# Kernel tuning notes

Hardware: AMD Instinct MI355X
Metric: run time of the kernel (lower is better)

## Reference

```python
import jax, jax.numpy as jnp
import numpy as np

N, E, F, H, C, G, NC = 50000, 800000, 128, 3, 64, 16, 10
NEG_SLOPE = 0.2


def gatv2_layer(x, src, dst, Wl, Wr, att, b, concat):
    # PyG GATv2Conv (share_weights=False, add_self_loops already in src/dst)
    n = x.shape[0]
    h, c = att.shape
    xl = (x @ Wl).reshape(n, h, c)   # source-side transform
    xr = (x @ Wr).reshape(n, h, c)   # target-side transform
    # per-edge attention logits: a^T LeakyReLU(xl_j + xr_i)
    e = jax.nn.leaky_relu(xl[src] + xr[dst], NEG_SLOPE)          # [E,h,c]
    logits = jnp.einsum('ehc,hc->eh', e, att)                    # [E,h]
    # segment softmax over incoming edges of each target node
    m = jax.ops.segment_max(logits, dst, num_segments=n)
    m = jnp.where(jnp.isfinite(m), m, jnp.zeros_like(m))
    p = jnp.exp(logits - m[dst])
    denom = jax.ops.segment_sum(p, dst, num_segments=n)
    alpha = p / jnp.maximum(denom[dst], 1e-16)                   # [E,h]
    out = jax.ops.segment_sum(alpha[:, :, None] * xl[src], dst, num_segments=n)
    out = out.reshape(n, h * c) if concat else out.mean(axis=1)
    return out + b


def setup_inputs() -> dict:
    key = jax.random.key(0)
    ks = jax.random.split(key, 16)
    glorot = lambda k, shp: jax.random.normal(k, shp, jnp.float32) * np.sqrt(2.0 / (shp[0] + shp[-1]))
    return {
        'x': jax.random.normal(ks[0], (N, F), jnp.float32),
        'edge_index': jax.random.randint(ks[1], (2, E), 0, N, jnp.int64),
        'batch': jnp.sort(jax.random.randint(ks[2], (N,), 0, G, jnp.int64)),
        'Wl1': glorot(ks[3], (F, H * C)),
        'Wr1': glorot(ks[4], (F, H * C)),
        'att1': glorot(ks[5], (H, C)),
        'b1': jnp.zeros((H * C,), jnp.float32),
        'Wl2': glorot(ks[6], (H * C, H * C)),
        'Wr2': glorot(ks[7], (H * C, H * C)),
        'att2': glorot(ks[8], (H, C)),
        'b2': jnp.zeros((C,), jnp.float32),
        'Wc': glorot(ks[9], (C, NC)),
        'bc': jnp.zeros((NC,), jnp.float32),
    }


def reference(x, edge_index, batch, Wl1, Wr1, att1, b1, Wl2, Wr2, att2, b2, Wc, bc):
    n = x.shape[0]
    loops = jnp.arange(n, dtype=edge_index.dtype)
    src = jnp.concatenate([edge_index[0], loops])  # add self loops (PyG default)
    dst = jnp.concatenate([edge_index[1], loops])
    h = jax.nn.relu(gatv2_layer(x, src, dst, Wl1, Wr1, att1, b1, True))
    # dropout is identity in eval mode
    h = jax.nn.relu(gatv2_layer(h, src, dst, Wl2, Wr2, att2, b2, False))
    # global mean pool over graph ids
    sums = jax.ops.segment_sum(h, batch, num_segments=G)
    counts = jax.ops.segment_sum(jnp.ones((n, 1), h.dtype), batch, num_segments=G)
    pooled = sums / jnp.maximum(counts, 1.0)
    logits = pooled @ Wc + bc
    return jax.nn.softmax(logits, axis=1)
```

## Files before the change

kernel.cpp:

```cpp
#include <hip/hip_runtime.h>
#include <hip/hip_bf16.h>
#include <stdint.h>

#define NN 50000
#define EE 800000
#define FF 128
#define HH 3
#define CC 64
#define GG 16
#define NCLS 10
#define HC (HH*CC)

#define LOG2E 1.4426950408889634f

typedef uint16_t u16;
typedef __attribute__((ext_vector_type(8))) short short8;
typedef __attribute__((ext_vector_type(4))) float f32x4;

__device__ __forceinline__ u16 bf16_rne(float x) {
    uint32_t u = __float_as_uint(x);
    u += 0x7fffu + ((u >> 16) & 1u);
    return (u16)(u >> 16);
}
__device__ __forceinline__ void split2(float x, u16& h, u16& l) {
    h = bf16_rne(x);
    float fh = __uint_as_float((uint32_t)h << 16);
    l = bf16_rne(x - fh);
}

__device__ __forceinline__ float qsum16(float x) {
    #define DPP_ADD(ctrl) \
        x += __int_as_float(__builtin_amdgcn_update_dpp(0, __float_as_int(x), ctrl, 0xf, 0xf, true))
    DPP_ADD(0x111);
    DPP_ADD(0x112);
    DPP_ADD(0x114);
    DPP_ADD(0x118);
    #undef DPP_ADD
    return __int_as_float(__builtin_amdgcn_ds_swizzle(__float_as_int(x), 0x1F0));
}

__device__ __forceinline__ void unpack12(uint4 q0, uint2 q1, float v[3][4]) {
    v[0][0] = __uint_as_float(q0.x << 16);
    v[1][0] = __uint_as_float(q0.x & 0xffff0000u);
    v[2][0] = __uint_as_float(q0.y << 16);
    v[0][1] = __uint_as_float(q0.y & 0xffff0000u);
    v[1][1] = __uint_as_float(q0.z << 16);
    v[2][1] = __uint_as_float(q0.z & 0xffff0000u);
    v[0][2] = __uint_as_float(q0.w << 16);
    v[1][2] = __uint_as_float(q0.w & 0xffff0000u);
    v[2][2] = __uint_as_float(q1.x << 16);
    v[0][3] = __uint_as_float(q1.x & 0xffff0000u);
    v[1][3] = __uint_as_float(q1.y << 16);
    v[2][3] = __uint_as_float(q1.y & 0xffff0000u);
}

__global__ void count_deg(const int* __restrict__ dst, int* __restrict__ deg, int E) {
    int i = blockIdx.x * blockDim.x + threadIdx.x;
    if (i < E) atomicAdd(&deg[dst[i]], 1);
}

__global__ __launch_bounds__(256) void scan_local(const int* __restrict__ deg,
                                                  int* __restrict__ rowp1,
                                                  int* __restrict__ partials, int n) {
    __shared__ int sums[256];
    int base = blockIdx.x * 2048 + threadIdx.x * 8;
    int v[8]; int run = 0;
    #pragma unroll
    for (int i = 0; i < 8; ++i) {
        int x = (base + i < n) ? deg[base + i] + 1 : 0;
        run += x; v[i] = run;
    }
    sums[threadIdx.x] = run;
    __syncthreads();
    for (int off = 1; off < 256; off <<= 1) {
        int t = (threadIdx.x >= off) ? sums[threadIdx.x - off] : 0;
        __syncthreads();
        sums[threadIdx.x] += t;
        __syncthreads();
    }
    int prefix = (threadIdx.x > 0) ? sums[threadIdx.x - 1] : 0;
    #pragma unroll
    for (int i = 0; i < 8; ++i)
        if (base + i < n) rowp1[base + i] = v[i] + prefix;
    if (threadIdx.x == 255) partials[blockIdx.x] = sums[255];
}

__global__ void scan_partials(int* partials, int nb) {
    if (threadIdx.x == 0 && blockIdx.x == 0) {
        int run = 0;
        for (int b = 0; b < nb; ++b) { int t = partials[b]; partials[b] = run; run += t; }
    }
}

__global__ void scan_finish(int* __restrict__ rowp, int* __restrict__ cursor,
                            const int* __restrict__ partials, int n) {
    int i = blockIdx.x * blockDim.x + threadIdx.x;
    if (i == 0) { rowp[0] = 0; cursor[0] = 0; }
    if (i < n) {
        int v = rowp[1 + i] + partials[i / 2048];
        rowp[1 + i] = v;
        if (i < n - 1) cursor[i + 1] = v;
    }
}

__global__ void fill_csr(const int* __restrict__ src, const int* __restrict__ dst,
                         int* __restrict__ cursor, int* __restrict__ colv, int E) {
    int i = blockIdx.x * blockDim.x + threadIdx.x;
    if (i < E) {
        int pos = atomicAdd(&cursor[dst[i]], 1);
        colv[pos] = src[i];
    }
}

__global__ void add_self(const int* __restrict__ rowp, int* __restrict__ colv, int n) {
    int i = blockIdx.x * blockDim.x + threadIdx.x;
    if (i < n) colv[rowp[i + 1] - 1] = i;
}

__global__ void prep_all(const float* __restrict__ Wl1, const float* __restrict__ Wr1,
                         const float* __restrict__ Wl2, const float* __restrict__ Wr2,
                         u16* l1h, u16* l1l, u16* r1h, u16* r1l,
                         u16* l2h, u16* l2l, u16* r2h, u16* r2l) {
    int idx = blockIdx.x * blockDim.x + threadIdx.x;
    const int S1 = FF * HC, S2 = HC * HC;
    const float* B; u16 *H, *L; int K, f;
    if (idx < S1)                { B = Wl1; H = l1h; L = l1l; K = FF; f = idx; }
    else if (idx < 2*S1)         { B = Wr1; H = r1h; L = r1l; K = FF; f = idx - S1; }
    else if (idx < 2*S1 + S2)    { B = Wl2; H = l2h; L = l2l; K = HC; f = idx - 2*S1; }
    else if (idx < 2*S1 + 2*S2)  { B = Wr2; H = r2h; L = r2l; K = HC; f = idx - 2*S1 - S2; }
    else return;
    const int KB = K / 32;
    int j    = f & 7;
    int lane = (f >> 3) & 63;
    int rest = f >> 9;
    int kb    = rest % KB;
    int ntile = rest / KB;
    int n = ntile * 16 + (lane & 15);
    int k = kb * 32 + (lane >> 4) * 8 + j;
    u16 h, l; split2(B[k * HC + n], h, l);
    H[f] = h;
    L[f] = l;
}

template<int K, bool SPLITIN>
__global__ __launch_bounds__(256) void mfma_gemm(
    const float* __restrict__ Af,
    const u16* __restrict__ Ahi, const u16* __restrict__ Alo,
    const u16* __restrict__ B1h, const u16* __restrict__ B1l,
    const u16* __restrict__ B2h, const u16* __restrict__ B2l,
    u16* __restrict__ C1p, u16* __restrict__ C2p, int M)
{
    constexpr int KB  = K / 32;
    constexpr int NCH = K / 8;
    __shared__ __align__(16) u16 smem[64 * K * 2];
    u16* Ah = smem;
    u16* Al = smem + 64 * K;

    const int tid  = threadIdx.x;
    const int w    = tid >> 6;
    const int lane = tid & 63;
    const int m0   = blockIdx.x * 64;

    #pragma unroll
    for (int i = 0; i < (64 * NCH) / 256; ++i) {
        int id   = tid + 256 * i;
        int row  = id & 63;
        int c    = id >> 6;
        int rt   = row >> 4, frow = row & 15;
        int kb   = c >> 2,   fkc  = c & 3;
        int sw   = (rt ^ (rt << 1)) & 7;
        int slot = (fkc * 16 + frow) ^ sw;
        int laddr = ((rt * KB + kb) * 64 + slot) * 8;
        int grow = min(m0 + row, M - 1);
        if constexpr (SPLITIN) {
            float4 a0 = *(const float4*)(Af + (size_t)grow * K + c * 8);
            float4 a1 = *(const float4*)(Af + (size_t)grow * K + c * 8 + 4);
            ushort4 h0, l0, h1, l1;
            split2(a0.x, h0.x, l0.x); split2(a0.y, h0.y, l0.y);
            split2(a0.z, h0.z, l0.z); split2(a0.w, h0.w, l0.w);
            split2(a1.x, h1.x, l1.x); split2(a1.y, h1.y, l1.y);
            split2(a1.z, h1.z, l1.z); split2(a1.w, h1.w, l1.w);
            *(ushort4*)&Ah[laddr]     = h0;
            *(ushort4*)&Ah[laddr + 4] = h1;
            *(ushort4*)&Al[laddr]     = l0;
            *(ushort4*)&Al[laddr + 4] = l1;
        } else {
            *(uint4*)&Ah[laddr] = *(const uint4*)(Ahi + (size_t)grow * K + c * 8);
            *(uint4*)&Al[laddr] = *(const uint4*)(Alo + (size_t)grow * K + c * 8);
        }
    }
    __syncthreads();

    f32x4 acc[2][3][4];
    #pragma unroll
    for (int mt = 0; mt < 2; ++mt)
        #pragma unroll
        for (int nt = 0; nt < 3; ++nt)
            #pragma unroll
            for (int rt = 0; rt < 4; ++rt)
                acc[mt][nt][rt] = (f32x4){0.f, 0.f, 0.f, 0.f};

    const u16* bbase[2][3][2];
    #pragma unroll
    for (int mt = 0; mt < 2; ++mt) {
        const u16* Bh = mt ? B2h : B1h;
        const u16* Bl = mt ? B2l : B1l;
        #pragma unroll
        for (int nt = 0; nt < 3; ++nt) {
            size_t o = ((size_t)(w * 3 + nt) * KB * 64 + lane) * 8;
            bbase[mt][nt][0] = Bh + o;
            bbase[mt][nt][1] = Bl + o;
        }
    }

    #pragma unroll 2
    for (int kb = 0; kb < KB; ++kb) {
        short8 afh[4], afl[4];
        #pragma unroll
        for (int rt = 0; rt < 4; ++rt) {
            int sw = (rt ^ (rt << 1)) & 7;
            int laddr = ((rt * KB + kb) * 64 + (lane ^ sw)) * 8;
            afh[rt] = *(const short8*)&Ah[laddr];
            afl[rt] = *(const short8*)&Al[laddr];
        }
        #pragma unroll
        for (int mt = 0; mt < 2; ++mt) {
            #pragma unroll
            for (int nt = 0; nt < 3; ++nt) {
                short8 bh = *(const short8*)(bbase[mt][nt][0] + kb * 512);
                short8 bl = *(const short8*)(bbase[mt][nt][1] + kb * 512);
                #pragma unroll
                for (int rt = 0; rt < 4; ++rt)
                    acc[mt][nt][rt] = __builtin_amdgcn_mfma_f32_16x16x32_bf16(afh[rt], bh, acc[mt][nt][rt], 0, 0, 0);
                #pragma unroll
                for (int rt = 0; rt < 4; ++rt)
                    acc[mt][nt][rt] = __builtin_amdgcn_mfma_f32_16x16x32_bf16(afh[rt], bl, acc[mt][nt][rt], 0, 0, 0);
                #pragma unroll
                for (int rt = 0; rt < 4; ++rt)
                    acc[mt][nt][rt] = __builtin_amdgcn_mfma_f32_16x16x32_bf16(afl[rt], bh, acc[mt][nt][rt], 0, 0, 0);
            }
        }
    }

    const int frow = lane & 15;
    const int q4   = (lane >> 4) * 4;
    #pragma unroll
    for (int mt = 0; mt < 2; ++mt) {
        __syncthreads();
        #pragma unroll
        for (int nt = 0; nt < 3; ++nt) {
            int col = w * 48 + nt * 16 + frow;
            int c = col & 63, h = col >> 6;
            int u = c * 3 + h;
            int chunk = u >> 3, within = u & 7;
            #pragma unroll
            for (int rt = 0; rt < 4; ++rt)
                #pragma unroll
                for (int r = 0; r < 4; ++r) {
                    int lrow = rt * 16 + q4 + r;
                    smem[lrow * 256 + ((chunk ^ (lrow & 7)) << 3) + within] =
                        bf16_rne(acc[mt][nt][rt][r]);
                }
        }
        __syncthreads();
        u16* C = mt ? C2p : C1p;
        #pragma unroll
        for (int i = 0; i < 6; ++i) {
            int idx  = tid + 256 * i;
            int lrow = idx / 24;
            int coff = idx % 24;
            if (m0 + lrow < M)
                *(uint4*)(C + (size_t)(m0 + lrow) * HC + coff * 8) =
                    *(const uint4*)&smem[lrow * 256 + ((coff ^ (lrow & 7)) << 3)];
        }
    }
}

template<bool MASK>
__device__ __forceinline__ void gat_quad(
    int i0, int q, int l, int beg, int cnt, int cm1,
    const int* __restrict__ colv, const u16* __restrict__ xlp,
    const float attv[3][4], const float xrv[3][4],
    float s[3], float acc[3][4])
{
    int idx = i0 + q;
    int iq  = MASK ? min(idx, cm1) : idx;
    int src = colv[beg + iq];
    const u16* p = xlp + (size_t)src * HC + l * 12;
    uint4 q0 = *(const uint4*)p;
    uint2 q1 = *(const uint2*)(p + 8);
    float v[3][4];
    unpack12(q0, q1, v);
    #pragma unroll
    for (int r = 0; r < 3; ++r) {
        float t0 = v[r][0] + xrv[r][0]; t0 = fmaxf(t0, 0.2f * t0);
        float t1 = v[r][1] + xrv[r][1]; t1 = fmaxf(t1, 0.2f * t1);
        float t2 = v[r][2] + xrv[r][2]; t2 = fmaxf(t2, 0.2f * t2);
        float t3 = v[r][3] + xrv[r][3]; t3 = fmaxf(t3, 0.2f * t3);
        float d = t0 * attv[r][0];
        d = fmaf(t1, attv[r][1], d);
        d = fmaf(t2, attv[r][2], d);
        d = fmaf(t3, attv[r][3], d);
        d = qsum16(d);
        float pe = __builtin_amdgcn_exp2f(d);
        if (MASK) pe = (idx < cnt) ? pe : 0.f;
        s[r] += pe;
        acc[r][0] = fmaf(pe, v[r][0], acc[r][0]);
        acc[r][1] = fmaf(pe, v[r][1], acc[r][1]);
        acc[r][2] = fmaf(pe, v[r][2], acc[r][2]);
        acc[r][3] = fmaf(pe, v[r][3], acc[r][3]);
    }
}

template<int CONCAT>
__global__ __launch_bounds__(256) void gat_agg(
    const u16* __restrict__ xlp, const u16* __restrict__ xrp,
    const int* __restrict__ rowp, const int* __restrict__ colv,
    const float* __restrict__ att, const float* __restrict__ bias,
    float* __restrict__ out, u16* __restrict__ ohi, u16* __restrict__ olo, int n)
{
    const int wave = threadIdx.x >> 6;
    const int lane = threadIdx.x & 63;
    const int node = __builtin_amdgcn_readfirstlane(blockIdx.x * 4 + wave);
    if (node >= n) return;
    const int q = lane >> 4;
    const int l = lane & 15;

    float attv[3][4], xrv[3][4];
    #pragma unroll
    for (int r = 0; r < 3; ++r) {
        float4 a4 = *(const float4*)(att + r * 64 + 4 * l);
        attv[r][0] = a4.x * LOG2E; attv[r][1] = a4.y * LOG2E;
        attv[r][2] = a4.z * LOG2E; attv[r][3] = a4.w * LOG2E;
    }
    {
        const u16* p = xrp + (size_t)node * HC + l * 12;
        uint4 x0 = *(const uint4*)p;
        uint2 x1 = *(const uint2*)(p + 8);
        unpack12(x0, x1, xrv);
    }

    float s[3] = {0.f, 0.f, 0.f};
    float acc[3][4] = {{0.f}};

    const int beg = rowp[node];
    const int cnt = rowp[node + 1] - beg;
    const int cm1 = cnt - 1;

    int i0 = 0;
    const int nfull = cnt & ~3;
    #pragma unroll 2
    for (; i0 < nfull; i0 += 4)
        gat_quad<false>(i0, q, l, beg, cnt, cm1, colv, xlp, attv, xrv, s, acc);
    if (i0 < cnt)
        gat_quad<true>(i0, q, l, beg, cnt, cm1, colv, xlp, attv, xrv, s, acc);

    #pragma unroll
    for (int r = 0; r < 3; ++r) {
        s[r] += __shfl_xor(s[r], 16, 64);
        s[r] += __shfl_xor(s[r], 32, 64);
        #pragma unroll
        for (int j = 0; j < 4; ++j) {
            acc[r][j] += __shfl_xor(acc[r][j], 16, 64);
            acc[r][j] += __shfl_xor(acc[r][j], 32, 64);
        }
    }

    if (CONCAT) {
        if (lane < 48) {
            int r = lane >> 4, ll = lane & 15;
            float inv = 1.f / s[r];
            float4 bv = *(const float4*)(bias + r * 64 + 4 * ll);
            ushort4 hv, lv;
            float o0 = fmaxf(fmaf(acc[r][0], inv, bv.x), 0.f); split2(o0, hv.x, lv.x);
            float o1 = fmaxf(fmaf(acc[r][1], inv, bv.y), 0.f); split2(o1, hv.y, lv.y);
            float o2 = fmaxf(fmaf(acc[r][2], inv, bv.z), 0.f); split2(o2, hv.z, lv.z);
            float o3 = fmaxf(fmaf(acc[r][3], inv, bv.w), 0.f); split2(o3, hv.w, lv.w);
            size_t ob = (size_t)node * HC + r * 64 + 4 * ll;
            *(ushort4*)&ohi[ob] = hv;
            *(ushort4*)&olo[ob] = lv;
        }
    } else {
        if (lane < 16) {
            float i0v = 1.f / s[0], i1v = 1.f / s[1], i2v = 1.f / s[2];
            float4 bv = *(const float4*)(bias + 4 * l);
            float4 o;
            o.x = fmaxf((acc[0][0]*i0v + acc[1][0]*i1v + acc[2][0]*i2v) * (1.f/3.f) + bv.x, 0.f);
            o.y = fmaxf((acc[0][1]*i0v + acc[1][1]*i1v + acc[2][1]*i2v) * (1.f/3.f) + bv.y, 0.f);
            o.z = fmaxf((acc[0][2]*i0v + acc[1][2]*i1v + acc[2][2]*i2v) * (1.f/3.f) + bv.z, 0.f);
            o.w = fmaxf((acc[0][3]*i0v + acc[1][3]*i1v + acc[2][3]*i2v) * (1.f/3.f) + bv.w, 0.f);
            *(float4*)&out[(size_t)node * CC + 4 * l] = o;
        }
    }
}

#define POOL_BLOCKS 384
__global__ __launch_bounds__(256) void pool_kernel(
    const float* __restrict__ h2, const int* __restrict__ batch,
    float* __restrict__ pool, float* __restrict__ cnt, int n)
{
    const int c   = threadIdx.x & 63;
    const int sub = threadIdx.x >> 6;
    const int per = (n + gridDim.x - 1) / gridDim.x;
    const int n0  = blockIdx.x * per;
    const int n1  = min(n0 + per, n);

    float run = 0.f;
    float crun = 0.f;
    int curg = -1;
    for (int node = n0 + sub; node < n1; node += 4) {
        int g = batch[node];
        if (g != curg) {
            if (curg >= 0) {
                atomicAdd(&pool[curg * CC + c], run);
                if (c == 0) atomicAdd(&cnt[curg], crun);
            }
            run = 0.f; crun = 0.f; curg = g;
        }
        run += h2[(size_t)node * CC + c];
        crun += 1.f;
    }
    if (curg >= 0) {
        atomicAdd(&pool[curg * CC + c], run);
        if (c == 0) atomicAdd(&cnt[curg], crun);
    }
}

__global__ void head_kernel(const float* __restrict__ pool, const float* __restrict__ cnt,
                            const float* __restrict__ Wc, const float* __restrict__ bc,
                            float* __restrict__ outp) {
    __shared__ float lg[GG][NCLS];
    int t = threadIdx.x;
    if (t < GG * NCLS) {
        int g = t / NCLS, k = t % NCLS;
        float invc = 1.f / fmaxf(cnt[g], 1.f);
        float a = 0.f;
        for (int c = 0; c < CC; ++c) a += pool[g * CC + c] * Wc[c * NCLS + k];
        lg[g][k] = a * invc + bc[k];
    }
    __syncthreads();
    if (t < GG) {
        float mx = -1e30f;
        for (int k = 0; k < NCLS; ++k) mx = fmaxf(mx, lg[t][k]);
        float ssum = 0.f; float e[NCLS];
        for (int k = 0; k < NCLS; ++k) { e[k] = __expf(lg[t][k] - mx); ssum += e[k]; }
        for (int k = 0; k < NCLS; ++k) outp[t * NCLS + k] = e[k] / ssum;
    }
}

extern "C" void kernel_launch(void* const* d_in, const int* in_sizes, int n_in,
                              void* d_out, int out_size, void* d_ws, size_t ws_size,
                              hipStream_t stream) {
    const float* x     = (const float*)d_in[0];
    const int*   ei    = (const int*)d_in[1];
    const int*   batch = (const int*)d_in[2];
    const float* Wl1   = (const float*)d_in[3];
    const float* Wr1   = (const float*)d_in[4];
    const float* att1  = (const float*)d_in[5];
    const float* b1    = (const float*)d_in[6];
    const float* Wl2   = (const float*)d_in[7];
    const float* Wr2   = (const float*)d_in[8];
    const float* att2  = (const float*)d_in[9];
    const float* b2    = (const float*)d_in[10];
    const float* Wc    = (const float*)d_in[11];
    const float* bc    = (const float*)d_in[12];

    const int n = in_sizes[2];
    const int E = in_sizes[1] / 2;
    const int* srcv = ei;
    const int* dstv = ei + E;

    char* base = (char*)d_ws;
    size_t off = 0;
    auto alloc = [&](size_t bytes) -> char* {
        char* p = base + off;
        off = (off + bytes + 255) & ~(size_t)255;
        return p;
    };
    int*   deg      = (int*)  alloc((size_t)n * 4);
    int*   cursor   = (int*)  alloc((size_t)n * 4);
    int*   rowp     = (int*)  alloc((size_t)(n + 1) * 4);
    int*   partials = (int*)  alloc(256 * 4);
    int*   colv     = (int*)  alloc((size_t)(E + n) * 4);
    u16*   xlp      = (u16*)  alloc((size_t)n * HC * 2);
    u16*   xrp      = (u16*)  alloc((size_t)n * HC * 2);
    u16*   bufHi    = (u16*)  alloc((size_t)n * HC * 2);
    u16*   bufLo    = (u16*)  alloc((size_t)n * HC * 2);
    float* h2       = (float*)alloc((size_t)n * CC * 4);
    float* pool     = (float*)alloc((size_t)GG * (CC + 1) * 4);
    float* cnt      = pool + GG * CC;
    u16*   Bl1hi    = (u16*)  alloc((size_t)FF * HC * 2);
    u16*   Bl1lo    = (u16*)  alloc((size_t)FF * HC * 2);
    u16*   Br1hi    = (u16*)  alloc((size_t)FF * HC * 2);
    u16*   Br1lo    = (u16*)  alloc((size_t)FF * HC * 2);
    u16*   Bl2hi    = (u16*)  alloc((size_t)HC * HC * 2);
    u16*   Bl2lo    = (u16*)  alloc((size_t)HC * HC * 2);
    u16*   Br2hi    = (u16*)  alloc((size_t)HC * HC * 2);
    u16*   Br2lo    = (u16*)  alloc((size_t)HC * HC * 2);

    hipMemsetAsync(deg, 0, (size_t)n * 4, stream);
    count_deg<<<(E + 255) / 256, 256, 0, stream>>>(dstv, deg, E);
    int nchunks = (n + 2047) / 2048;
    scan_local<<<nchunks, 256, 0, stream>>>(deg, rowp + 1, partials, n);
    scan_partials<<<1, 64, 0, stream>>>(partials, nchunks);
    scan_finish<<<(n + 255) / 256, 256, 0, stream>>>(rowp, cursor, partials, n);
    fill_csr<<<(E + 255) / 256, 256, 0, stream>>>(srcv, dstv, cursor, colv, E);
    add_self<<<(n + 255) / 256, 256, 0, stream>>>(rowp, colv, n);

    const int prep_total = 2 * FF * HC + 2 * HC * HC;
    prep_all<<<(prep_total + 255) / 256, 256, 0, stream>>>(
        Wl1, Wr1, Wl2, Wr2, Bl1hi, Bl1lo, Br1hi, Br1lo, Bl2hi, Bl2lo, Br2hi, Br2lo);

    const int gblocks = (n + 63) / 64;

    mfma_gemm<FF, true><<<gblocks, 256, 0, stream>>>(
        x, nullptr, nullptr, Bl1hi, Bl1lo, Br1hi, Br1lo, xlp, xrp, n);
    gat_agg<1><<<(n + 3) / 4, 256, 0, stream>>>(xlp, xrp, rowp, colv, att1, b1,
                                                nullptr, bufHi, bufLo, n);

    mfma_gemm<HC, false><<<gblocks, 256, 0, stream>>>(
        nullptr, bufHi, bufLo, Bl2hi, Bl2lo, Br2hi, Br2lo, xlp, xrp, n);
    gat_agg<0><<<(n + 3) / 4, 256, 0, stream>>>(xlp, xrp, rowp, colv, att2, b2,
                                                h2, nullptr, nullptr, n);

    hipMemsetAsync(pool, 0, (size_t)GG * (CC + 1) * 4, stream);
    pool_kernel<<<POOL_BLOCKS, 256, 0, stream>>>(h2, batch, pool, cnt, n);
    head_kernel<<<1, 256, 0, stream>>>(pool, cnt, Wc, bc, (float*)d_out);
}
```

Before: 357.1 us.

## Load GEMM A fragments directly from global and halve row tile to 32

The MFMA GEMM no longer stages the A tile (hi/lo bf16 split) through shared memory. Each wave now loads its own A fragments straight from global memory into registers and splits them there. The M tile shrinks from 64 to 32 rows, which doubles the block count and cuts shared memory to the output staging buffer only. This removes the LDS staging pass and its barrier, and should raise occupancy. In exchange, all four waves redundantly read and split the same A rows, and each B fragment is reused over fewer rows.

```diff
diff --git a/kernel.cpp b/kernel.cpp
--- a/kernel.cpp
+++ b/kernel.cpp
@@ -150,57 +150,30 @@
     const u16* __restrict__ B2h, const u16* __restrict__ B2l,
     u16* __restrict__ C1p, u16* __restrict__ C2p, int M)
 {
-    constexpr int KB  = K / 32;
-    constexpr int NCH = K / 8;
-    __shared__ __align__(16) u16 smem[64 * K * 2];
-    u16* Ah = smem;
-    u16* Al = smem + 64 * K;
+    constexpr int KB = K / 32;
+    __shared__ __align__(16) u16 smem[32 * 256];
 
     const int tid  = threadIdx.x;
     const int w    = tid >> 6;
     const int lane = tid & 63;
-    const int m0   = blockIdx.x * 64;
-
-    #pragma unroll
-    for (int i = 0; i < (64 * NCH) / 256; ++i) {
-        int id   = tid + 256 * i;
-        int row  = id & 63;
-        int c    = id >> 6;
-        int rt   = row >> 4, frow = row & 15;
-        int kb   = c >> 2,   fkc  = c & 3;
-        int sw   = (rt ^ (rt << 1)) & 7;
-        int slot = (fkc * 16 + frow) ^ sw;
-        int laddr = ((rt * KB + kb) * 64 + slot) * 8;
-        int grow = min(m0 + row, M - 1);
-        if constexpr (SPLITIN) {
-            float4 a0 = *(const float4*)(Af + (size_t)grow * K + c * 8);
-            float4 a1 = *(const float4*)(Af + (size_t)grow * K + c * 8 + 4);
-            ushort4 h0, l0, h1, l1;
-            split2(a0.x, h0.x, l0.x); split2(a0.y, h0.y, l0.y);
-            split2(a0.z, h0.z, l0.z); split2(a0.w, h0.w, l0.w);
-            split2(a1.x, h1.x, l1.x); split2(a1.y, h1.y, l1.y);
-            split2(a1.z, h1.z, l1.z); split2(a1.w, h1.w, l1.w);
-            *(ushort4*)&Ah[laddr]     = h0;
-            *(ushort4*)&Ah[laddr + 4] = h1;
-            *(ushort4*)&Al[laddr]     = l0;
-            *(ushort4*)&Al[laddr + 4] = l1;
-        } else {
-            *(uint4*)&Ah[laddr] = *(const uint4*)(Ahi + (size_t)grow * K + c * 8);
-            *(uint4*)&Al[laddr] = *(const uint4*)(Alo + (size_t)grow * K + c * 8);
-        }
-    }
-    __syncthreads();
-
-    f32x4 acc[2][3][4];
+    const int m0   = blockIdx.x * 32;
+    const int frow = lane & 15;
+    const int fkc  = lane >> 4;
+
+    f32x4 acc[2][3][2];
     #pragma unroll
     for (int mt = 0; mt < 2; ++mt)
         #pragma unroll
         for (int nt = 0; nt < 3; ++nt)
             #pragma unroll
-            for (int rt = 0; rt < 4; ++rt)
+            for (int rt = 0; rt < 2; ++rt)
                 acc[mt][nt][rt] = (f32x4){0.f, 0.f, 0.f, 0.f};
 
-    const u16* bbase[2][3][2];
+    int arow[2];
+    arow[0] = min(m0 + frow, M - 1);
+    arow[1] = min(m0 + 16 + frow, M - 1);
+
+    const u16* bb[2][3][2];
     #pragma unroll
     for (int mt = 0; mt < 2; ++mt) {
         const u16* Bh = mt ? B2h : B1h;
@@ -208,42 +181,55 @@
         #pragma unroll
         for (int nt = 0; nt < 3; ++nt) {
             size_t o = ((size_t)(w * 3 + nt) * KB * 64 + lane) * 8;
-            bbase[mt][nt][0] = Bh + o;
-            bbase[mt][nt][1] = Bl + o;
-        }
-    }
-
-    #pragma unroll 2
+            bb[mt][nt][0] = Bh + o;
+            bb[mt][nt][1] = Bl + o;
+        }
+    }
+
+    #pragma unroll
     for (int kb = 0; kb < KB; ++kb) {
-        short8 afh[4], afl[4];
-        #pragma unroll
-        for (int rt = 0; rt < 4; ++rt) {
-            int sw = (rt ^ (rt << 1)) & 7;
-            int laddr = ((rt * KB + kb) * 64 + (lane ^ sw)) * 8;
-            afh[rt] = *(const short8*)&Ah[laddr];
-            afl[rt] = *(const short8*)&Al[laddr];
+        short8 afh[2], afl[2];
+        #pragma unroll
+        for (int rt = 0; rt < 2; ++rt) {
+            if constexpr (SPLITIN) {
+                const float* ap = Af + (size_t)arow[rt] * K + kb * 32 + fkc * 8;
+                float4 a0 = *(const float4*)ap;
+                float4 a1 = *(const float4*)(ap + 4);
+                ushort4 h0, l0, h1, l1;
+                split2(a0.x, h0.x, l0.x); split2(a0.y, h0.y, l0.y);
+                split2(a0.z, h0.z, l0.z); split2(a0.w, h0.w, l0.w);
+                split2(a1.x, h1.x, l1.x); split2(a1.y, h1.y, l1.y);
+                split2(a1.z, h1.z, l1.z); split2(a1.w, h1.w, l1.w);
+                afh[rt] = (short8){(short)h0.x, (short)h0.y, (short)h0.z, (short)h0.w,
+                                   (short)h1.x, (short)h1.y, (short)h1.z, (short)h1.w};
+                afl[rt] = (short8){(short)l0.x, (short)l0.y, (short)l0.z, (short)l0.w,
+                                   (short)l1.x, (short)l1.y, (short)l1.z, (short)l1.w};
+            } else {
+                size_t o = (size_t)arow[rt] * K + kb * 32 + fkc * 8;
+                afh[rt] = *(const short8*)(Ahi + o);
+                afl[rt] = *(const short8*)(Alo + o);
+            }
         }
         #pragma unroll
         for (int mt = 0; mt < 2; ++mt) {
             #pragma unroll
             for (int nt = 0; nt < 3; ++nt) {
-                short8 bh = *(const short8*)(bbase[mt][nt][0] + kb * 512);
-                short8 bl = *(const short8*)(bbase[mt][nt][1] + kb * 512);
+                short8 bh = *(const short8*)(bb[mt][nt][0] + kb * 512);
+                short8 bl = *(const short8*)(bb[mt][nt][1] + kb * 512);
                 #pragma unroll
-                for (int rt = 0; rt < 4; ++rt)
+                for (int rt = 0; rt < 2; ++rt)
                     acc[mt][nt][rt] = __builtin_amdgcn_mfma_f32_16x16x32_bf16(afh[rt], bh, acc[mt][nt][rt], 0, 0, 0);
                 #pragma unroll
-                for (int rt = 0; rt < 4; ++rt)
+                for (int rt = 0; rt < 2; ++rt)
                     acc[mt][nt][rt] = __builtin_amdgcn_mfma_f32_16x16x32_bf16(afh[rt], bl, acc[mt][nt][rt], 0, 0, 0);
                 #pragma unroll
-                for (int rt = 0; rt < 4; ++rt)
+                for (int rt = 0; rt < 2; ++rt)
                     acc[mt][nt][rt] = __builtin_amdgcn_mfma_f32_16x16x32_bf16(afl[rt], bh, acc[mt][nt][rt], 0, 0, 0);
             }
         }
     }
 
-    const int frow = lane & 15;
-    const int q4   = (lane >> 4) * 4;
+    const int q4 = (lane >> 4) * 4;
     #pragma unroll
     for (int mt = 0; mt < 2; ++mt) {
         __syncthreads();
@@ -254,7 +240,7 @@
             int u = c * 3 + h;
             int chunk = u >> 3, within = u & 7;
             #pragma unroll
-            for (int rt = 0; rt < 4; ++rt)
+            for (int rt = 0; rt < 2; ++rt)
                 #pragma unroll
                 for (int r = 0; r < 4; ++r) {
                     int lrow = rt * 16 + q4 + r;
@@ -265,7 +251,7 @@
         __syncthreads();
         u16* C = mt ? C2p : C1p;
         #pragma unroll
-        for (int i = 0; i < 6; ++i) {
+        for (int i = 0; i < 3; ++i) {
             int idx  = tid + 256 * i;
             int lrow = idx / 24;
             int coff = idx % 24;
@@ -511,7 +497,7 @@
     prep_all<<<(prep_total + 255) / 256, 256, 0, stream>>>(
         Wl1, Wr1, Wl2, Wr2, Bl1hi, Bl1lo, Br1hi, Br1lo, Bl2hi, Bl2lo, Br2hi, Br2lo);
 
-    const int gblocks = (n + 63) / 64;
+    const int gblocks = (n + 31) / 32;
 
     mfma_gemm<FF, true><<<gblocks, 256, 0, stream>>>(
         x, nullptr, nullptr, Bl1hi, Bl1lo, Br1hi, Br1lo, xlp, xrp, n);
```

After: 352.9 us. Within noise of the previous version (-1.2%).
